# Kernel tuning notes

Measured on AMD Instinct MI355X. Metric: run time of the kernel, lower is better.

## Reference

```python
import jax, jax.numpy as jnp
import numpy as np

B, L, D, H = 4, 2048, 1024, 64  # batch, seq, d_model, head_size

def setup_inputs() -> dict:
    key = jax.random.key(0)
    k1, k2 = jax.random.split(key)
    x = jax.random.normal(k1, (B, L, D), dtype=jnp.float32)
    # nn.Linear(d_model, head_size, bias=False) weight: [head_size, d_model]
    Wq = jax.random.normal(k2, (H, D), dtype=jnp.float32) * (1.0 / np.sqrt(D))
    return {"x": x, "Wq": Wq}

def reference(x, Wq):
    # Faithful to source bug: q, k, v ALL use the query projection.
    q = jnp.einsum('bld,hd->blh', x, Wq)
    k = q
    v = q
    d_k = x.shape[-1]  # source uses d_model, not head_size
    scores = jnp.einsum('blh,bmh->blm', q, k) / jnp.sqrt(jnp.float32(d_k))
    Lq = x.shape[1]
    causal = jnp.tril(jnp.ones((Lq, Lq), dtype=bool))
    scores = jnp.where(causal, scores, -jnp.inf)
    attn = jax.nn.softmax(scores, axis=-1)
    # dropout in eval mode -> identity
    return jnp.einsum('blm,bmh->blh', attn, v)
```

## Files before the change

kernel.cpp:

```cpp
#include <hip/hip_runtime.h>
#include <cmath>

#define Bb 4
#define Ll 2048
#define Dd 1024
#define Hh 64

typedef float f32x4 __attribute__((ext_vector_type(4)));
typedef short s16x8 __attribute__((ext_vector_type(8)));

__device__ __forceinline__ unsigned short f2bf(float f) {
    union { float f; unsigned int u; } v; v.f = f;
    unsigned int u = v.u;
    return (unsigned short)((u + 0x7FFFu + ((u >> 16) & 1u)) >> 16);
}
__device__ __forceinline__ unsigned int pack2(float a, float b) {
    return (unsigned int)f2bf(a) | ((unsigned int)f2bf(b) << 16);
}

__global__ __launch_bounds__(256) void wq_cvt(const float* __restrict__ Wq,
                                              unsigned short* __restrict__ wqb) {
    const int i = (blockIdx.x * 256 + threadIdx.x) * 8;
    float4 a = *(const float4*)(Wq + i);
    float4 b = *(const float4*)(Wq + i + 4);
    uint4 p; p.x = pack2(a.x, a.y); p.y = pack2(a.z, a.w);
    p.z = pack2(b.x, b.y); p.w = pack2(b.z, b.w);
    *(uint4*)(wqb + i) = p;
}

__global__ __launch_bounds__(256, 2) void proj_mfma(const float* __restrict__ x,
                                                    const unsigned short* __restrict__ wqb,
                                                    unsigned short* __restrict__ q,
                                                    unsigned short* __restrict__ qT) {
    __shared__ uint4 xs4[32 * 16];
    __shared__ uint4 ws4[32 * 64];
    const int t = threadIdx.x;
    const int lane = t & 63;
    const int w = t >> 6;
    const int m15 = lane & 15;
    const int q_ = lane >> 4;
    const int row0 = blockIdx.x * 16;

    f32x4 acc = {0.f, 0.f, 0.f, 0.f};

    for (int k0 = 0; k0 < Dd; k0 += 256) {
        __syncthreads();
#pragma unroll
        for (int j = 0; j < 2; ++j) {
            int idx = t + j * 256;
            int r = idx >> 5, kc = idx & 31;
            const float* src = x + (size_t)(row0 + r) * Dd + k0 + kc * 8;
            float4 a = *(const float4*)src;
            float4 b = *(const float4*)(src + 4);
            uint4 p; p.x = pack2(a.x, a.y); p.y = pack2(a.z, a.w);
            p.z = pack2(b.x, b.y); p.w = pack2(b.z, b.w);
            xs4[kc * 16 + (r ^ (kc & 15))] = p;
        }
#pragma unroll
        for (int j = 0; j < 8; ++j) {
            int idx = t + j * 256;
            int h = idx >> 5, kc = idx & 31;
            ws4[kc * 64 + (h ^ kc)] = *(const uint4*)(wqb + (size_t)h * Dd + k0 + kc * 8);
        }
        __syncthreads();
#pragma unroll
        for (int ks = 0; ks < 8; ++ks) {
            int kc = ks * 4 + q_;
            s16x8 A = *(const s16x8*)&xs4[kc * 16 + (m15 ^ (kc & 15))];
            s16x8 B = *(const s16x8*)&ws4[kc * 64 + ((w * 16 + m15) ^ kc)];
            acc = __builtin_amdgcn_mfma_f32_16x16x32_bf16(A, B, acc, 0, 0, 0);
        }
    }
    const int h = w * 16 + m15;
    const int b = row0 >> 11;
    const int mloc = (row0 & 2047) + q_ * 4;
    unsigned short u0 = f2bf(acc[0]), u1 = f2bf(acc[1]), u2 = f2bf(acc[2]), u3 = f2bf(acc[3]);
    q[(size_t)(row0 + q_ * 4 + 0) * Hh + h] = u0;
    q[(size_t)(row0 + q_ * 4 + 1) * Hh + h] = u1;
    q[(size_t)(row0 + q_ * 4 + 2) * Hh + h] = u2;
    q[(size_t)(row0 + q_ * 4 + 3) * Hh + h] = u3;
    ushort4 pk; pk.x = u0; pk.y = u1; pk.z = u2; pk.w = u3;
    *(ushort4*)&qT[((size_t)(b * Hh + h)) * Ll + mloc] = pk;
}

__global__ __launch_bounds__(256, 3) void flash_mfma(const unsigned short* __restrict__ qg,
                                                     const unsigned short* __restrict__ qTg,
                                                     float* __restrict__ PO,
                                                     float* __restrict__ ML) {
    const int qt = blockIdx.x;
    const int s  = blockIdx.y;
    const int b  = blockIdx.z;
    if (s > (qt >> 2)) return;
    __shared__ uint4 Qs4[512], Ks4[512], Vt4[512];
    __shared__ __align__(16) unsigned short Pb[4 * 16 * 72];
    const int t = threadIdx.x, lane = t & 63, w = t >> 6;
    const int m15 = lane & 15, q_ = lane >> 4;
    const unsigned short* qb  = qg  + (size_t)b * Ll * Hh;
    const unsigned short* qTb = qTg + (size_t)b * Hh * Ll;

#pragma unroll
    for (int j = 0; j < 2; ++j) {
        int idx = t + j * 256;
        int r = idx >> 3, hc = idx & 7;
        Qs4[hc * 64 + (r ^ hc)] = *(const uint4*)(qb + (size_t)(qt * 64 + r) * Hh + hc * 8);
    }
    f32x4 Oacc[4];
#pragma unroll
    for (int i = 0; i < 4; ++i) Oacc[i] = (f32x4){0.f, 0.f, 0.f, 0.f};
    float mr = -INFINITY, lr = 0.f;
    const int n_it = min(4, qt - 4 * s + 1);
    const int c_base = s * 256;
    const int row = qt * 64 + w * 16 + m15;
    unsigned short* Pr = Pb + (w * 16 + m15) * 72;

    for (int it = 0; it < n_it; ++it) {
        const int c0 = c_base + it * 64;
        __syncthreads();
#pragma unroll
        for (int j = 0; j < 2; ++j) {
            int idx = t + j * 256;
            int c = idx >> 3, hc = idx & 7;
            Ks4[hc * 64 + (c ^ hc)] = *(const uint4*)(qb + (size_t)(c0 + c) * Hh + hc * 8);
        }
#pragma unroll
        for (int j = 0; j < 2; ++j) {
            int idx = t + j * 256;
            int h = idx >> 3, cc = idx & 7;
            Vt4[cc * 64 + (h ^ cc)] = *(const uint4*)(qTb + (size_t)h * Ll + c0 + cc * 8);
        }
        __syncthreads();
        f32x4 sc[4];
#pragma unroll
        for (int ct = 0; ct < 4; ++ct) sc[ct] = (f32x4){0.f, 0.f, 0.f, 0.f};
#pragma unroll
        for (int ks = 0; ks < 2; ++ks) {
            int hc = ks * 4 + q_;
            s16x8 Bq = *(const s16x8*)&Qs4[hc * 64 + ((w * 16 + m15) ^ hc)];
#pragma unroll
            for (int ct = 0; ct < 4; ++ct) {
                s16x8 Ak = *(const s16x8*)&Ks4[hc * 64 + ((ct * 16 + m15) ^ hc)];
                sc[ct] = __builtin_amdgcn_mfma_f32_16x16x32_bf16(Ak, Bq, sc[ct], 0, 0, 0);
            }
        }
        const bool diag = (4 * s + it) == qt;
        float v[16];
#pragma unroll
        for (int ct = 0; ct < 4; ++ct)
#pragma unroll
            for (int r = 0; r < 4; ++r) {
                float sv = sc[ct][r] * 0.03125f;
                if (diag && (c0 + ct * 16 + q_ * 4 + r > row)) sv = -INFINITY;
                v[ct * 4 + r] = sv;
            }
        float vmax = v[0];
#pragma unroll
        for (int i = 1; i < 16; ++i) vmax = fmaxf(vmax, v[i]);
        vmax = fmaxf(vmax, __shfl_xor(vmax, 16, 64));
        vmax = fmaxf(vmax, __shfl_xor(vmax, 32, 64));
        float mnew = fmaxf(mr, vmax);
        float alpha = __expf(mr - mnew);
        float p[16];
        float psum = 0.f;
#pragma unroll
        for (int i = 0; i < 16; ++i) { p[i] = __expf(v[i] - mnew); psum += p[i]; }
        psum += __shfl_xor(psum, 16, 64);
        psum += __shfl_xor(psum, 32, 64);
        lr = lr * alpha + psum;
        mr = mnew;
#pragma unroll
        for (int ht = 0; ht < 4; ++ht) Oacc[ht] *= alpha;
#pragma unroll
        for (int ct = 0; ct < 4; ++ct) {
            uint2 pr; pr.x = pack2(p[ct * 4 + 0], p[ct * 4 + 1]);
            pr.y = pack2(p[ct * 4 + 2], p[ct * 4 + 3]);
            *(uint2*)(Pr + ct * 16 + q_ * 4) = pr;
        }
#pragma unroll
        for (int kc = 0; kc < 2; ++kc) {
            int cc = kc * 4 + q_;
            s16x8 Bp = *(const s16x8*)(Pr + kc * 32 + q_ * 8);
#pragma unroll
            for (int ht = 0; ht < 4; ++ht) {
                s16x8 Av = *(const s16x8*)&Vt4[cc * 64 + ((ht * 16 + m15) ^ cc)];
                Oacc[ht] = __builtin_amdgcn_mfma_f32_16x16x32_bf16(Av, Bp, Oacc[ht], 0, 0, 0);
            }
        }
    }
    const size_t base = ((size_t)((b * 32 + qt) * 8 + s)) * 4096;
#pragma unroll
    for (int ht = 0; ht < 4; ++ht)
        *(f32x4*)&PO[base + (size_t)(w * 16 + m15) * 64 + ht * 16 + q_ * 4] = Oacc[ht];
    if (q_ == 0) {
        float* mlp = ML + ((size_t)((b * 32 + qt) * 8 + s)) * 128;
        mlp[(w * 16 + m15) * 2 + 0] = mr;
        mlp[(w * 16 + m15) * 2 + 1] = lr;
    }
}

__global__ __launch_bounds__(256) void combine_k(const float* __restrict__ PO,
                                                 const float* __restrict__ ML,
                                                 float* __restrict__ out) {
    const int bq = blockIdx.x;
    const int b = bq >> 5, qt = bq & 31;
    const int ns = (qt >> 2) + 1;
    const int t = threadIdx.x;
    const int r = blockIdx.y * 32 + (t >> 3);
    const int c8 = (t & 7) * 8;
    const float* mlp = ML + (size_t)bq * 8 * 128;
    const float* pob = PO + (size_t)bq * 8 * 4096;
    float M = -INFINITY;
    for (int si = 0; si < ns; ++si) M = fmaxf(M, mlp[si * 128 + r * 2]);
    float L = 0.f;
    f32x4 a0 = {0.f, 0.f, 0.f, 0.f}, a1 = a0;
    for (int si = 0; si < ns; ++si) {
        float ms = mlp[si * 128 + r * 2], ls = mlp[si * 128 + r * 2 + 1];
        float wgt = __expf(ms - M);
        L += ls * wgt;
        const f32x4* sp = (const f32x4*)(pob + (size_t)si * 4096 + r * 64 + c8);
        a0 += wgt * sp[0];
        a1 += wgt * sp[1];
    }
    float inv = 1.0f / L;
    f32x4* op = (f32x4*)(out + (size_t)(b * Ll + qt * 64 + r) * 64 + c8);
    op[0] = a0 * inv;
    op[1] = a1 * inv;
}

extern "C" void kernel_launch(void* const* d_in, const int* in_sizes, int n_in,
                              void* d_out, int out_size, void* d_ws, size_t ws_size,
                              hipStream_t stream) {
    const float* x  = (const float*)d_in[0];
    const float* Wq = (const float*)d_in[1];
    float* out = (float*)d_out;
    char* ws = (char*)d_ws;
    unsigned short* q   = (unsigned short*)ws;
    unsigned short* qT  = (unsigned short*)(ws + (1 << 20));
    float* PO = (float*)(ws + (2 << 20));
    float* ML = (float*)(ws + (18 << 20));
    unsigned short* wqb = (unsigned short*)(ws + (19 << 20));

    wq_cvt<<<32, 256, 0, stream>>>(Wq, wqb);
    proj_mfma<<<512, 256, 0, stream>>>(x, wqb, q, qT);
    flash_mfma<<<dim3(32, 8, Bb), 256, 0, stream>>>(q, qT, PO, ML);
    combine_k<<<dim3(128, 2), 256, 0, stream>>>(PO, ML, out);
}
```

Before: 101.6 us.

## Rewrite projection without LDS, compact flash grid, use exp2 softmax

The projection kernel drops shared-memory staging and its syncs. Each wave now reads x rows and bf16 Wq directly from global memory and computes all 64 head columns across four accumulators, using 128-thread blocks. The flash kernel launches only the 144 valid (qt, split) pairs per batch and decodes them with a triangular-index formula, so no blocks start only to exit early. Softmax uses hardware exp2 with log2(e) folded into the scale, and the combine step uses exp2 to match. Risks are weaker reuse of Wq across waves in the projection and a small index-decoding cost per block.

Measured after the change: 103.2 us. No clear change (+1.6%).

```diff
diff --git a/kernel.cpp b/kernel.cpp
--- a/kernel.cpp
+++ b/kernel.cpp
@@ -8,6 +8,13 @@
 
 typedef float f32x4 __attribute__((ext_vector_type(4)));
 typedef short s16x8 __attribute__((ext_vector_type(8)));
+
+#if __has_builtin(__builtin_amdgcn_exp2f)
+#define EXP2(x) __builtin_amdgcn_exp2f(x)
+#else
+#define EXP2(x) exp2f(x)
+#endif
+#define SCL 0.0450842200278f
 
 __device__ __forceinline__ unsigned short f2bf(float f) {
     union { float f; unsigned int u; } v; v.f = f;
@@ -28,69 +35,63 @@
     *(uint4*)(wqb + i) = p;
 }
 
-__global__ __launch_bounds__(256, 2) void proj_mfma(const float* __restrict__ x,
-                                                    const unsigned short* __restrict__ wqb,
-                                                    unsigned short* __restrict__ q,
-                                                    unsigned short* __restrict__ qT) {
-    __shared__ uint4 xs4[32 * 16];
-    __shared__ uint4 ws4[32 * 64];
+__global__ __launch_bounds__(128) void proj_mfma(const float* __restrict__ x,
+                                                 const unsigned short* __restrict__ wqb,
+                                                 unsigned short* __restrict__ q,
+                                                 unsigned short* __restrict__ qT) {
     const int t = threadIdx.x;
     const int lane = t & 63;
-    const int w = t >> 6;
-    const int m15 = lane & 15;
-    const int q_ = lane >> 4;
-    const int row0 = blockIdx.x * 16;
-
-    f32x4 acc = {0.f, 0.f, 0.f, 0.f};
-
-    for (int k0 = 0; k0 < Dd; k0 += 256) {
-        __syncthreads();
-#pragma unroll
-        for (int j = 0; j < 2; ++j) {
-            int idx = t + j * 256;
-            int r = idx >> 5, kc = idx & 31;
-            const float* src = x + (size_t)(row0 + r) * Dd + k0 + kc * 8;
-            float4 a = *(const float4*)src;
-            float4 b = *(const float4*)(src + 4);
-            uint4 p; p.x = pack2(a.x, a.y); p.y = pack2(a.z, a.w);
-            p.z = pack2(b.x, b.y); p.w = pack2(b.z, b.w);
-            xs4[kc * 16 + (r ^ (kc & 15))] = p;
-        }
-#pragma unroll
-        for (int j = 0; j < 8; ++j) {
-            int idx = t + j * 256;
-            int h = idx >> 5, kc = idx & 31;
-            ws4[kc * 64 + (h ^ kc)] = *(const uint4*)(wqb + (size_t)h * Dd + k0 + kc * 8);
-        }
-        __syncthreads();
-#pragma unroll
-        for (int ks = 0; ks < 8; ++ks) {
-            int kc = ks * 4 + q_;
-            s16x8 A = *(const s16x8*)&xs4[kc * 16 + (m15 ^ (kc & 15))];
-            s16x8 B = *(const s16x8*)&ws4[kc * 64 + ((w * 16 + m15) ^ kc)];
-            acc = __builtin_amdgcn_mfma_f32_16x16x32_bf16(A, B, acc, 0, 0, 0);
-        }
-    }
-    const int h = w * 16 + m15;
+    const int wv = t >> 6;
+    const int m15 = lane & 15, q_ = lane >> 4;
+    const int row0 = blockIdx.x * 32 + wv * 16;
+    const float* xr = x + (size_t)(row0 + m15) * Dd + q_ * 8;
+
+    f32x4 acc[4];
+#pragma unroll
+    for (int i = 0; i < 4; ++i) acc[i] = (f32x4){0.f, 0.f, 0.f, 0.f};
+
+#pragma unroll 4
+    for (int ks = 0; ks < 32; ++ks) {
+        float4 a = *(const float4*)(xr + ks * 32);
+        float4 b = *(const float4*)(xr + ks * 32 + 4);
+        union { s16x8 v; uint4 u; } A;
+        A.u.x = pack2(a.x, a.y); A.u.y = pack2(a.z, a.w);
+        A.u.z = pack2(b.x, b.y); A.u.w = pack2(b.z, b.w);
+#pragma unroll
+        for (int ct = 0; ct < 4; ++ct) {
+            s16x8 B = *(const s16x8*)(wqb + (size_t)(ct * 16 + m15) * Dd + ks * 32 + q_ * 8);
+            acc[ct] = __builtin_amdgcn_mfma_f32_16x16x32_bf16(A.v, B, acc[ct], 0, 0, 0);
+        }
+    }
     const int b = row0 >> 11;
     const int mloc = (row0 & 2047) + q_ * 4;
-    unsigned short u0 = f2bf(acc[0]), u1 = f2bf(acc[1]), u2 = f2bf(acc[2]), u3 = f2bf(acc[3]);
-    q[(size_t)(row0 + q_ * 4 + 0) * Hh + h] = u0;
-    q[(size_t)(row0 + q_ * 4 + 1) * Hh + h] = u1;
-    q[(size_t)(row0 + q_ * 4 + 2) * Hh + h] = u2;
-    q[(size_t)(row0 + q_ * 4 + 3) * Hh + h] = u3;
-    ushort4 pk; pk.x = u0; pk.y = u1; pk.z = u2; pk.w = u3;
-    *(ushort4*)&qT[((size_t)(b * Hh + h)) * Ll + mloc] = pk;
+#pragma unroll
+    for (int ct = 0; ct < 4; ++ct) {
+        const int h = ct * 16 + m15;
+        unsigned short u0 = f2bf(acc[ct][0]), u1 = f2bf(acc[ct][1]);
+        unsigned short u2 = f2bf(acc[ct][2]), u3 = f2bf(acc[ct][3]);
+        q[(size_t)(row0 + q_ * 4 + 0) * Hh + h] = u0;
+        q[(size_t)(row0 + q_ * 4 + 1) * Hh + h] = u1;
+        q[(size_t)(row0 + q_ * 4 + 2) * Hh + h] = u2;
+        q[(size_t)(row0 + q_ * 4 + 3) * Hh + h] = u3;
+        ushort4 pk; pk.x = u0; pk.y = u1; pk.z = u2; pk.w = u3;
+        *(ushort4*)&qT[((size_t)(b * Hh + h)) * Ll + mloc] = pk;
+    }
 }
 
 __global__ __launch_bounds__(256, 3) void flash_mfma(const unsigned short* __restrict__ qg,
                                                      const unsigned short* __restrict__ qTg,
                                                      float* __restrict__ PO,
                                                      float* __restrict__ ML) {
-    const int qt = blockIdx.x;
-    const int s  = blockIdx.y;
-    const int b  = blockIdx.z;
-    if (s > (qt >> 2)) return;
+    const int i = blockIdx.x;
+    const int b = blockIdx.y;
+    int g = (int)((sqrtf(1.0f + 2.0f * (float)i) - 1.0f) * 0.5f);
+    while (2 * g * (g + 1) > i) --g;
+    while (2 * (g + 1) * (g + 2) <= i) ++g;
+    const int r_ = i - 2 * g * (g + 1);
+    const int qt = 4 * g + r_ / (g + 1);
+    const int s  = r_ % (g + 1);
+
     __shared__ uint4 Qs4[512], Ks4[512], Vt4[512];
     __shared__ __align__(16) unsigned short Pb[4 * 16 * 72];
     const int t = threadIdx.x, lane = t & 63, w = t >> 6;
@@ -106,7 +107,7 @@
     }
     f32x4 Oacc[4];
 #pragma unroll
-    for (int i = 0; i < 4; ++i) Oacc[i] = (f32x4){0.f, 0.f, 0.f, 0.f};
+    for (int k = 0; k < 4; ++k) Oacc[k] = (f32x4){0.f, 0.f, 0.f, 0.f};
     float mr = -INFINITY, lr = 0.f;
     const int n_it = min(4, qt - 4 * s + 1);
     const int c_base = s * 256;
@@ -148,21 +149,21 @@
         for (int ct = 0; ct < 4; ++ct)
 #pragma unroll
             for (int r = 0; r < 4; ++r) {
-                float sv = sc[ct][r] * 0.03125f;
+                float sv = sc[ct][r] * SCL;
                 if (diag && (c0 + ct * 16 + q_ * 4 + r > row)) sv = -INFINITY;
                 v[ct * 4 + r] = sv;
             }
         float vmax = v[0];
 #pragma unroll
-        for (int i = 1; i < 16; ++i) vmax = fmaxf(vmax, v[i]);
+        for (int k = 1; k < 16; ++k) vmax = fmaxf(vmax, v[k]);
         vmax = fmaxf(vmax, __shfl_xor(vmax, 16, 64));
         vmax = fmaxf(vmax, __shfl_xor(vmax, 32, 64));
         float mnew = fmaxf(mr, vmax);
-        float alpha = __expf(mr - mnew);
+        float alpha = EXP2(mr - mnew);
         float p[16];
         float psum = 0.f;
 #pragma unroll
-        for (int i = 0; i < 16; ++i) { p[i] = __expf(v[i] - mnew); psum += p[i]; }
+        for (int k = 0; k < 16; ++k) { p[k] = EXP2(v[k] - mnew); psum += p[k]; }
         psum += __shfl_xor(psum, 16, 64);
         psum += __shfl_xor(psum, 32, 64);
         lr = lr * alpha + psum;
@@ -201,7 +202,8 @@
                                                  const float* __restrict__ ML,
                                                  float* __restrict__ out) {
     const int bq = blockIdx.x;
-    const int b = bq >> 5, qt = bq & 31;
+    const int qt = bq & 31;
+    const int b = bq >> 5;
     const int ns = (qt >> 2) + 1;
     const int t = threadIdx.x;
     const int r = blockIdx.y * 32 + (t >> 3);
@@ -214,7 +216,7 @@
     f32x4 a0 = {0.f, 0.f, 0.f, 0.f}, a1 = a0;
     for (int si = 0; si < ns; ++si) {
         float ms = mlp[si * 128 + r * 2], ls = mlp[si * 128 + r * 2 + 1];
-        float wgt = __expf(ms - M);
+        float wgt = EXP2(ms - M);
         L += ls * wgt;
         const f32x4* sp = (const f32x4*)(pob + (size_t)si * 4096 + r * 64 + c8);
         a0 += wgt * sp[0];
@@ -240,7 +242,7 @@
     unsigned short* wqb = (unsigned short*)(ws + (19 << 20));
 
     wq_cvt<<<32, 256, 0, stream>>>(Wq, wqb);
-    proj_mfma<<<512, 256, 0, stream>>>(x, wqb, q, qT);
-    flash_mfma<<<dim3(32, 8, Bb), 256, 0, stream>>>(q, qT, PO, ML);
+    proj_mfma<<<256, 128, 0, stream>>>(x, wqb, q, qT);
+    flash_mfma<<<dim3(144, Bb), 256, 0, stream>>>(q, qT, PO, ML);
     combine_k<<<dim3(128, 2), 256, 0, stream>>>(PO, ML, out);
 }
```
